# Performance work log

Hardware: AMD Instinct MI355X
Metric: run time of the kernel (lower is better)

Reference implementation:

```python
import jax, jax.numpy as jnp
import numpy as np

N_NODES = 200000
N_EDGES = 6400000
N_LAYERS = 3
Z_DIM = 4  # 2*4 + 1 + 3 == 12 == Linear in_features


def setup_inputs() -> dict:
    key = jax.random.key(0)
    ks = jax.random.split(key, 7)
    z = jax.random.normal(ks[0], (N_NODES, Z_DIM), dtype=jnp.float32)
    r = jax.random.uniform(ks[1], (N_EDGES, 1), dtype=jnp.float32)
    r_hat = jax.random.normal(ks[2], (N_EDGES, 3), dtype=jnp.float32)
    # Per-layer Linear(12, 1) weights and biases, stacked over layers.
    W = jax.random.normal(ks[3], (N_LAYERS, 1, 12), dtype=jnp.float32) * (1.0 / np.sqrt(12.0))
    b = jnp.zeros((N_LAYERS, 1), dtype=jnp.float32)
    src = jax.random.randint(ks[4], (N_EDGES,), 0, N_NODES, dtype=jnp.int32)
    dst = jax.random.randint(ks[5], (N_EDGES,), 0, N_NODES, dtype=jnp.int32)
    return {"z": z, "r": r, "r_hat": r_hat, "W": W, "b": b, "src": src, "dst": dst}


def reference(z, r, r_hat, W, b, src, dst):
    # batch['x'] = batch['z'].copy()
    x = z
    n_nodes = z.shape[0]
    for i in range(W.shape[0]):
        # Per-edge gather + concat -> [E, 12]
        inpt = jnp.concatenate([z[src], z[dst], r, r_hat], axis=-1)
        # Tiny Linear(12, 1) -> per-edge scalar message [E, 1]
        msg = inpt @ W[i].T + b[i]
        # Scatter-sum messages onto destination nodes, residual update.
        agg = jax.ops.segment_sum(msg, dst, num_segments=n_nodes)  # [N, 1]
        z = z + agg  # broadcast over the 4 node features
    return z, x
```

## Files before the change

kernel.cpp:

```cpp
#include <hip/hip_runtime.h>

#define N_NODES 200000
#define N_EDGES 6400000
#define K_BUCKETS 64
#define BUCKET 3125
#define NSB 3200
#define CHUNK 2000
#define P_SPLIT 8

__device__ __forceinline__ unsigned short f2bf(float x) {
    unsigned u = __float_as_uint(x);
    u += 0x7fffu + ((u >> 16) & 1u);
    return (unsigned short)(u >> 16);
}
__device__ __forceinline__ float bf2f(unsigned short h) {
    return __uint_as_float((unsigned)h << 16);
}


__global__ __launch_bounds__(256) void prep_kernel(
    const float4* __restrict__ z, float4* __restrict__ x_out,
    const float* __restrict__ W,
    float* __restrict__ u, float* __restrict__ v)
{
    int n = blockIdx.x * 256 + threadIdx.x;
    if (n >= N_NODES) return;
    float4 zv = z[n];
    x_out[n] = zv;
    float a0 = W[0], a1 = W[1], a2 = W[2], a3 = W[3];
    float q0 = W[4], q1 = W[5], q2 = W[6], q3 = W[7];
    u[n] = a0 * zv.x + a1 * zv.y + a2 * zv.z + a3 * zv.w;
    v[n] = q0 * zv.x + q1 * zv.y + q2 * zv.z + q3 * zv.w;
}

__global__ __launch_bounds__(256) void hist_kernel(const int* __restrict__ dst,
                                                   int* __restrict__ counts)
{
    __shared__ int cnt[K_BUCKETS];
    int tid = threadIdx.x, sb = blockIdx.x;
    if (tid < K_BUCKETS) cnt[tid] = 0;
    __syncthreads();
    int e0 = sb * CHUNK;
    for (int i = tid; i < CHUNK; i += 256)
        atomicAdd(&cnt[dst[e0 + i] / BUCKET], 1);
    __syncthreads();
    if (tid < K_BUCKETS) counts[sb * K_BUCKETS + tid] = cnt[tid];
}

__global__ __launch_bounds__(256) void scan_cols(const int* __restrict__ counts,
                                                 int* __restrict__ baseRel,
                                                 int* __restrict__ tot)
{
    __shared__ int buf[256];
    __shared__ int carry_s;
    int k = blockIdx.x, tid = threadIdx.x;
    if (tid == 0) carry_s = 0;
    __syncthreads();
    for (int base = 0; base < NSB; base += 256) {
        int idx = base + tid;
        int v = (idx < NSB) ? counts[idx * K_BUCKETS + k] : 0;
        buf[tid] = v;
        __syncthreads();
        for (int off = 1; off < 256; off <<= 1) {
            int t = (tid >= off) ? buf[tid - off] : 0;
            __syncthreads();
            buf[tid] += t;
            __syncthreads();
        }
        int incl = buf[tid];
        if (idx < NSB) baseRel[idx * K_BUCKETS + k] = carry_s + incl - v;
        __syncthreads();
        if (tid == 255) carry_s += incl;
        __syncthreads();
    }
    if (tid == 255) tot[k] = carry_s;
}

__global__ __launch_bounds__(64) void scan_tot(const int* __restrict__ tot,
                                               int* __restrict__ bstart)
{
    __shared__ int buf[K_BUCKETS];
    int tid = threadIdx.x;
    int v = tot[tid];
    buf[tid] = v;
    __syncthreads();
    for (int off = 1; off < K_BUCKETS; off <<= 1) {
        int t = (tid >= off) ? buf[tid - off] : 0;
        __syncthreads();
        buf[tid] += t;
        __syncthreads();
    }
    bstart[tid] = buf[tid] - v;
    if (tid == K_BUCKETS - 1) bstart[K_BUCKETS] = buf[tid];
}

__global__ __launch_bounds__(256) void scatter_kernel(
    const int* __restrict__ src, const int* __restrict__ dst,
    const float* __restrict__ r, const float* __restrict__ r_hat,
    const float* __restrict__ W, const float* __restrict__ b,
    const int* __restrict__ counts, const int* __restrict__ baseRel,
    const int* __restrict__ bstart,
    int* __restrict__ packedA, unsigned short* __restrict__ c0a,
    unsigned short* __restrict__ c1a, unsigned short* __restrict__ c2a)
{
    __shared__ int cur[K_BUCKETS];
    __shared__ int delta[K_BUCKETS];
    __shared__ int scanbuf[K_BUCKETS];
    __shared__ int            lpack[CHUNK];
    __shared__ unsigned short lc0[CHUNK];
    __shared__ unsigned short lc1[CHUNK];
    __shared__ unsigned short lc2[CHUNK];
    __shared__ unsigned char  skb[CHUNK];

    int tid = threadIdx.x, sb = blockIdx.x;

    if (tid < K_BUCKETS) {
        int v = counts[sb * K_BUCKETS + tid];
        scanbuf[tid] = v;
    }
    __syncthreads();
    for (int off = 1; off < K_BUCKETS; off <<= 1) {
        int t = 0;
        if (tid < K_BUCKETS && tid >= off) t = scanbuf[tid - off];
        __syncthreads();
        if (tid < K_BUCKETS) scanbuf[tid] += t;
        __syncthreads();
    }
    if (tid < K_BUCKETS) {
        int v = counts[sb * K_BUCKETS + tid];
        int localBase = scanbuf[tid] - v;
        int gBase = bstart[tid] + baseRel[sb * K_BUCKETS + tid];
        delta[tid] = gBase - localBase;
        cur[tid] = localBase;
    }
    __syncthreads();

    float w8_0 = W[8],  w9_0 = W[9],  w10_0 = W[10], w11_0 = W[11], b0 = b[0];
    float w8_1 = W[20], w9_1 = W[21], w10_1 = W[22], w11_1 = W[23], b1 = b[1];
    float w8_2 = W[32], w9_2 = W[33], w10_2 = W[34], w11_2 = W[35], b2 = b[2];

    int e0 = sb * CHUNK;
    for (int i = tid; i < CHUNK; i += 256) {
        int e = e0 + i;
        int d = dst[e];
        int k = d / BUCKET;
        int dl = d - k * BUCKET;
        int slot = atomicAdd(&cur[k], 1);
        int sn = src[e];
        float rv = r[e];
        size_t he = 3 * (size_t)e;
        float h0 = r_hat[he], h1 = r_hat[he + 1], h2 = r_hat[he + 2];
        lpack[slot] = (sn << 12) | dl;
        lc0[slot] = f2bf(w8_0 * rv + w9_0 * h0 + w10_0 * h1 + w11_0 * h2 + b0);
        lc1[slot] = f2bf(w8_1 * rv + w9_1 * h0 + w10_1 * h1 + w11_1 * h2 + b1);
        lc2[slot] = f2bf(w8_2 * rv + w9_2 * h0 + w10_2 * h1 + w11_2 * h2 + b2);
        skb[slot] = (unsigned char)k;
    }
    __syncthreads();

    for (int s = tid; s < CHUNK; s += 256) {
        int k = skb[s];
        int gpos = delta[k] + s;
        packedA[gpos] = lpack[s];
        c0a[gpos] = lc0[s];
        c1a[gpos] = lc1[s];
        c2a[gpos] = lc2[s];
    }
}

__global__ __launch_bounds__(1024) void pagg_kernel(
    const int* __restrict__ packedA, const unsigned short* __restrict__ ca,
    const int* __restrict__ bstart,
    const float* __restrict__ u, const float* __restrict__ v,
    float* __restrict__ partial)
{
    __shared__ float vsl[BUCKET];
    __shared__ float aggsl[BUCKET];
    int tid = threadIdx.x, blk = blockIdx.x;
    int k = blk / P_SPLIT;
    int p = blk - k * P_SPLIT;
    int nbase = k * BUCKET;

    for (int i = tid; i < BUCKET; i += 1024) {
        aggsl[i] = 0.0f;
        vsl[i] = v[nbase + i];
    }
    __syncthreads();

    int estart = bstart[k], eend = bstart[k + 1];
    int len = eend - estart;
    int per = (len + P_SPLIT - 1) / P_SPLIT;
    int lo = estart + p * per;
    int hi = min(lo + per, eend);

    for (int j = lo + tid; j < hi; j += 1024) {
        int pack = packedA[j];
        int s = pack >> 12;
        int dl = pack & 4095;
        float c = bf2f(ca[j]);
        unsafeAtomicAdd(&aggsl[dl], u[s] + vsl[dl] + c);
    }
    __syncthreads();

    float* pout = partial + (size_t)blk * BUCKET;
    for (int i = tid; i < BUCKET; i += 1024) pout[i] = aggsl[i];
}

__global__ __launch_bounds__(256) void fin_kernel(
    const float4* __restrict__ z0, const float* __restrict__ partial,
    const float* __restrict__ Sin, float* __restrict__ Sout,
    const float* __restrict__ W, int layer,
    float* __restrict__ u, float* __restrict__ v, float4* __restrict__ z_out)
{
    int n = blockIdx.x * 256 + threadIdx.x;
    if (n >= N_NODES) return;
    int k = n / BUCKET;
    int i = n - k * BUCKET;
    float agg = 0.0f;
    const float* pk = partial + (size_t)k * P_SPLIT * BUCKET + i;
#pragma unroll
    for (int p = 0; p < P_SPLIT; ++p) agg += pk[(size_t)p * BUCKET];
    float S = ((layer == 0) ? 0.0f : Sin[n]) + agg;
    if (layer < 2) {
        const float* Wn = W + 12 * (layer + 1);
        float a0 = Wn[0], a1 = Wn[1], a2 = Wn[2], a3 = Wn[3];
        float q0 = Wn[4], q1 = Wn[5], q2 = Wn[6], q3 = Wn[7];
        float A = a0 + a1 + a2 + a3, B = q0 + q1 + q2 + q3;
        float4 zv = z0[n];
        Sout[n] = S;
        u[n] = a0 * zv.x + a1 * zv.y + a2 * zv.z + a3 * zv.w + A * S;
        v[n] = q0 * zv.x + q1 * zv.y + q2 * zv.z + q3 * zv.w + B * S;
    } else {
        float4 zv = z0[n];
        zv.x += S; zv.y += S; zv.z += S; zv.w += S;
        z_out[n] = zv;
    }
}


__global__ __launch_bounds__(256) void init_kernel(
    const float4* __restrict__ z_in, float4* __restrict__ z_cur,
    float4* __restrict__ x_out, float* __restrict__ agg)
{
    int n = blockIdx.x * blockDim.x + threadIdx.x;
    if (n < N_NODES) {
        float4 vv = z_in[n];
        z_cur[n] = vv; x_out[n] = vv; agg[n] = 0.0f;
    }
}

__global__ __launch_bounds__(256) void edge_kernel(
    const float* __restrict__ z, const float* __restrict__ r,
    const float* __restrict__ r_hat, const int* __restrict__ src,
    const int* __restrict__ dst, const float* __restrict__ Wl,
    const float* __restrict__ bl, float* __restrict__ agg)
{
    int e = blockIdx.x * blockDim.x + threadIdx.x;
    if (e >= N_EDGES) return;
    float w0 = Wl[0], w1 = Wl[1], w2 = Wl[2], w3 = Wl[3];
    float w4 = Wl[4], w5 = Wl[5], w6 = Wl[6], w7 = Wl[7];
    float w8 = Wl[8], w9 = Wl[9], w10 = Wl[10], w11 = Wl[11];
    float bias = bl[0];
    int s = src[e], d = dst[e];
    float4 zs = ((const float4*)z)[s];
    float4 zd = ((const float4*)z)[d];
    float rv = r[e];
    const float* rh = r_hat + 3 * (size_t)e;
    float msg = w0*zs.x + w1*zs.y + w2*zs.z + w3*zs.w
              + w4*zd.x + w5*zd.y + w6*zd.z + w7*zd.w
              + w8*rv + w9*rh[0] + w10*rh[1] + w11*rh[2] + bias;
    unsafeAtomicAdd(&agg[d], msg);
}

__global__ __launch_bounds__(256) void node_update(float4* __restrict__ z_cur,
                                                   float* __restrict__ agg)
{
    int n = blockIdx.x * blockDim.x + threadIdx.x;
    if (n < N_NODES) {
        float a = agg[n]; float4 vv = z_cur[n];
        vv.x += a; vv.y += a; vv.z += a; vv.w += a;
        z_cur[n] = vv; agg[n] = 0.0f;
    }
}

__global__ __launch_bounds__(256) void final_update(const float4* __restrict__ z_cur,
                                                    const float* __restrict__ agg,
                                                    float4* __restrict__ z_out)
{
    int n = blockIdx.x * blockDim.x + threadIdx.x;
    if (n < N_NODES) {
        float a = agg[n]; float4 vv = z_cur[n];
        vv.x += a; vv.y += a; vv.z += a; vv.w += a;
        z_out[n] = vv;
    }
}


extern "C" void kernel_launch(void* const* d_in, const int* in_sizes, int n_in,
                              void* d_out, int out_size, void* d_ws, size_t ws_size,
                              hipStream_t stream)
{
    const float* z     = (const float*)d_in[0];
    const float* r     = (const float*)d_in[1];
    const float* r_hat = (const float*)d_in[2];
    const float* W     = (const float*)d_in[3];
    const float* b     = (const float*)d_in[4];
    const int*   src   = (const int*)d_in[5];
    const int*   dst   = (const int*)d_in[6];
    float* out = (float*)d_out;

    char* ws = (char*)d_ws;
    size_t off = 0;
    auto alloc = [&](size_t bytes) {
        void* p = ws + off;
        off += (bytes + 15) & ~(size_t)15;
        return p;
    };
    int*            packedA = (int*)alloc((size_t)N_EDGES * 4);
    unsigned short* c0a     = (unsigned short*)alloc((size_t)N_EDGES * 2);
    unsigned short* c1a     = (unsigned short*)alloc((size_t)N_EDGES * 2);
    unsigned short* c2a     = (unsigned short*)alloc((size_t)N_EDGES * 2);
    int*            counts  = (int*)alloc((size_t)NSB * K_BUCKETS * 4);
    int*            baseRel = (int*)alloc((size_t)NSB * K_BUCKETS * 4);
    int*            tot     = (int*)alloc((size_t)K_BUCKETS * 4);
    int*            bstart  = (int*)alloc((size_t)(K_BUCKETS + 1) * 4);
    float*          Sa      = (float*)alloc((size_t)N_NODES * 4);
    float*          Sb      = (float*)alloc((size_t)N_NODES * 4);
    float*          ubuf    = (float*)alloc((size_t)N_NODES * 4);
    float*          vbuf    = (float*)alloc((size_t)N_NODES * 4);
    float*          partial = (float*)alloc((size_t)K_BUCKETS * P_SPLIT * BUCKET * 4);
    size_t required = off;

    dim3 nblk((N_NODES + 255) / 256);

    if (ws_size >= required) {
        prep_kernel<<<nblk, 256, 0, stream>>>(
            (const float4*)z, (float4*)(out + 4 * (size_t)N_NODES), W, ubuf, vbuf);
        hist_kernel<<<NSB, 256, 0, stream>>>(dst, counts);
        scan_cols<<<K_BUCKETS, 256, 0, stream>>>(counts, baseRel, tot);
        scan_tot<<<1, 64, 0, stream>>>(tot, bstart);
        scatter_kernel<<<NSB, 256, 0, stream>>>(src, dst, r, r_hat, W, b,
                                                counts, baseRel, bstart,
                                                packedA, c0a, c1a, c2a);
        pagg_kernel<<<K_BUCKETS * P_SPLIT, 1024, 0, stream>>>(
            packedA, c0a, bstart, ubuf, vbuf, partial);
        fin_kernel<<<nblk, 256, 0, stream>>>(
            (const float4*)z, partial, Sa, Sa, W, 0, ubuf, vbuf, (float4*)out);
        pagg_kernel<<<K_BUCKETS * P_SPLIT, 1024, 0, stream>>>(
            packedA, c1a, bstart, ubuf, vbuf, partial);
        fin_kernel<<<nblk, 256, 0, stream>>>(
            (const float4*)z, partial, Sa, Sb, W, 1, ubuf, vbuf, (float4*)out);
        pagg_kernel<<<K_BUCKETS * P_SPLIT, 1024, 0, stream>>>(
            packedA, c2a, bstart, ubuf, vbuf, partial);
        fin_kernel<<<nblk, 256, 0, stream>>>(
            (const float4*)z, partial, Sb, Sb, W, 2, ubuf, vbuf, (float4*)out);
    } else {
        float* agg   = (float*)d_ws;
        float* z_cur = agg + N_NODES;
        dim3 eblk((N_EDGES + 255) / 256);
        init_kernel<<<nblk, 256, 0, stream>>>(
            (const float4*)z, (float4*)z_cur,
            (float4*)(out + 4 * (size_t)N_NODES), agg);
        for (int i = 0; i < 3; ++i) {
            edge_kernel<<<eblk, 256, 0, stream>>>(
                z_cur, r, r_hat, src, dst, W + 12 * i, b + i, agg);
            if (i < 2)
                node_update<<<nblk, 256, 0, stream>>>((float4*)z_cur, agg);
            else
                final_update<<<nblk, 256, 0, stream>>>(
                    (const float4*)z_cur, agg, (float4*)out);
        }
    }
}
```

Baseline: 373.6 us.

## Add second-level sort of edges by source bucket for gather locality

Adds a second counting-sort pass (histogram, scan, scatter) that reorders edges within each destination bucket by source-node bucket, so the u[s] gathers in the aggregation kernels hit nearby addresses. The partial-split factor is lowered from 8 to 4 when the extra workspace is available. This trades one extra full pass over the 6.4M edge arrays and more workspace for better cache locality across the three aggregation launches. A fallback keeps the old path when workspace is insufficient.

```diff
diff --git a/kernel.cpp b/kernel.cpp
--- a/kernel.cpp
+++ b/kernel.cpp
@@ -6,7 +6,7 @@
 #define BUCKET 3125
 #define NSB 3200
 #define CHUNK 2000
-#define P_SPLIT 8
+#define CPB 64
 
 __device__ __forceinline__ unsigned short f2bf(float x) {
     unsigned u = __float_as_uint(x);
@@ -114,10 +114,7 @@
 
     int tid = threadIdx.x, sb = blockIdx.x;
 
-    if (tid < K_BUCKETS) {
-        int v = counts[sb * K_BUCKETS + tid];
-        scanbuf[tid] = v;
-    }
+    if (tid < K_BUCKETS) scanbuf[tid] = counts[sb * K_BUCKETS + tid];
     __syncthreads();
     for (int off = 1; off < K_BUCKETS; off <<= 1) {
         int t = 0;
@@ -168,17 +165,132 @@
     }
 }
 
+
+__global__ __launch_bounds__(256) void hist2_kernel(
+    const int* __restrict__ packedA, const int* __restrict__ bstart,
+    int* __restrict__ counts2)
+{
+    __shared__ int cnt[K_BUCKETS];
+    int tid = threadIdx.x, blk = blockIdx.x;
+    int k = blk >> 6, ci = blk & 63;
+    if (tid < K_BUCKETS) cnt[tid] = 0;
+    __syncthreads();
+    int lo = bstart[k] + ci * CHUNK;
+    int hi = min(lo + CHUNK, bstart[k + 1]);
+    for (int j = lo + tid; j < hi; j += 256)
+        atomicAdd(&cnt[(packedA[j] >> 12) / BUCKET], 1);
+    __syncthreads();
+    if (tid < K_BUCKETS) counts2[blk * K_BUCKETS + tid] = cnt[tid];
+}
+
+__global__ __launch_bounds__(256) void scan2_kernel(
+    const int* __restrict__ counts2, int* __restrict__ baseRel2)
+{
+    __shared__ int m[CPB * K_BUCKETS];
+    __shared__ int colT[K_BUCKETS];
+    __shared__ int colB[K_BUCKETS];
+    int k = blockIdx.x, tid = threadIdx.x;
+    for (int i = tid; i < CPB * K_BUCKETS; i += 256)
+        m[i] = counts2[k * CPB * K_BUCKETS + i];
+    __syncthreads();
+    if (tid < K_BUCKETS) {
+        int s = tid, t = 0;
+        for (int ci = 0; ci < CPB; ++ci) {
+            int v = m[ci * K_BUCKETS + s];
+            m[ci * K_BUCKETS + s] = t;
+            t += v;
+        }
+        colT[s] = t;
+    }
+    __syncthreads();
+    if (tid == 0) {
+        int t = 0;
+        for (int s = 0; s < K_BUCKETS; ++s) { colB[s] = t; t += colT[s]; }
+    }
+    __syncthreads();
+    for (int i = tid; i < CPB * K_BUCKETS; i += 256) {
+        int s = i & 63;
+        baseRel2[k * CPB * K_BUCKETS + i] = colB[s] + m[i];
+    }
+}
+
+__global__ __launch_bounds__(256) void scatter2_kernel(
+    const int* __restrict__ packedA,
+    const unsigned short* __restrict__ c0a, const unsigned short* __restrict__ c1a,
+    const unsigned short* __restrict__ c2a,
+    const int* __restrict__ bstart, const int* __restrict__ counts2,
+    const int* __restrict__ baseRel2,
+    int* __restrict__ packedB,
+    unsigned short* __restrict__ c0b, unsigned short* __restrict__ c1b,
+    unsigned short* __restrict__ c2b)
+{
+    __shared__ int cur[K_BUCKETS];
+    __shared__ int delta[K_BUCKETS];
+    __shared__ int scanbuf[K_BUCKETS];
+    __shared__ int            lpack[CHUNK];
+    __shared__ unsigned short lc0[CHUNK];
+    __shared__ unsigned short lc1[CHUNK];
+    __shared__ unsigned short lc2[CHUNK];
+    __shared__ unsigned char  skb[CHUNK];
+
+    int tid = threadIdx.x, blk = blockIdx.x;
+    int k = blk >> 6, ci = blk & 63;
+    int lo = bstart[k] + ci * CHUNK;
+    int hi = min(lo + CHUNK, bstart[k + 1]);
+    int n = hi - lo;
+    if (n <= 0) return;
+
+    if (tid < K_BUCKETS) scanbuf[tid] = counts2[blk * K_BUCKETS + tid];
+    __syncthreads();
+    for (int off = 1; off < K_BUCKETS; off <<= 1) {
+        int t = 0;
+        if (tid < K_BUCKETS && tid >= off) t = scanbuf[tid - off];
+        __syncthreads();
+        if (tid < K_BUCKETS) scanbuf[tid] += t;
+        __syncthreads();
+    }
+    if (tid < K_BUCKETS) {
+        int v = counts2[blk * K_BUCKETS + tid];
+        int localBase = scanbuf[tid] - v;
+        int gBase = bstart[k] + baseRel2[blk * K_BUCKETS + tid];
+        delta[tid] = gBase - localBase;
+        cur[tid] = localBase;
+    }
+    __syncthreads();
+
+    for (int j = lo + tid; j < hi; j += 256) {
+        int pack = packedA[j];
+        int s = (pack >> 12) / BUCKET;
+        int slot = atomicAdd(&cur[s], 1);
+        lpack[slot] = pack;
+        lc0[slot] = c0a[j];
+        lc1[slot] = c1a[j];
+        lc2[slot] = c2a[j];
+        skb[slot] = (unsigned char)s;
+    }
+    __syncthreads();
+
+    for (int t = tid; t < n; t += 256) {
+        int s = skb[t];
+        int g = delta[s] + t;
+        packedB[g] = lpack[t];
+        c0b[g] = lc0[t];
+        c1b[g] = lc1[t];
+        c2b[g] = lc2[t];
+    }
+}
+
 __global__ __launch_bounds__(1024) void pagg_kernel(
-    const int* __restrict__ packedA, const unsigned short* __restrict__ ca,
+    const int* __restrict__ packed, const unsigned short* __restrict__ ca,
     const int* __restrict__ bstart,
     const float* __restrict__ u, const float* __restrict__ v,
-    float* __restrict__ partial)
+    float* __restrict__ partial, int ps)
 {
     __shared__ float vsl[BUCKET];
     __shared__ float aggsl[BUCKET];
     int tid = threadIdx.x, blk = blockIdx.x;
-    int k = blk / P_SPLIT;
-    int p = blk - k * P_SPLIT;
+    int k = blk / ps;
+    int p = blk - k * ps;
     int nbase = k * BUCKET;
 
     for (int i = tid; i < BUCKET; i += 1024) {
@@ -189,16 +301,15 @@
 
     int estart = bstart[k], eend = bstart[k + 1];
     int len = eend - estart;
-    int per = (len + P_SPLIT - 1) / P_SPLIT;
+    int per = (len + ps - 1) / ps;
     int lo = estart + p * per;
     int hi = min(lo + per, eend);
 
     for (int j = lo + tid; j < hi; j += 1024) {
-        int pack = packedA[j];
+        int pack = packed[j];
         int s = pack >> 12;
         int dl = pack & 4095;
-        float c = bf2f(ca[j]);
-        unsafeAtomicAdd(&aggsl[dl], u[s] + vsl[dl] + c);
+        unsafeAtomicAdd(&aggsl[dl], u[s] + vsl[dl] + bf2f(ca[j]));
     }
     __syncthreads();
 
@@ -209,7 +320,7 @@
 __global__ __launch_bounds__(256) void fin_kernel(
     const float4* __restrict__ z0, const float* __restrict__ partial,
     const float* __restrict__ Sin, float* __restrict__ Sout,
-    const float* __restrict__ W, int layer,
+    const float* __restrict__ W, int layer, int ps,
     float* __restrict__ u, float* __restrict__ v, float4* __restrict__ z_out)
 {
     int n = blockIdx.x * 256 + threadIdx.x;
@@ -217,9 +328,8 @@
     int k = n / BUCKET;
     int i = n - k * BUCKET;
     float agg = 0.0f;
-    const float* pk = partial + (size_t)k * P_SPLIT * BUCKET + i;
-#pragma unroll
-    for (int p = 0; p < P_SPLIT; ++p) agg += pk[(size_t)p * BUCKET];
+    const float* pk = partial + (size_t)k * ps * BUCKET + i;
+    for (int p = 0; p < ps; ++p) agg += pk[(size_t)p * BUCKET];
     float S = ((layer == 0) ? 0.0f : Sin[n]) + agg;
     if (layer < 2) {
         const float* Wn = W + 12 * (layer + 1);
@@ -328,12 +438,20 @@
     float*          Sb      = (float*)alloc((size_t)N_NODES * 4);
     float*          ubuf    = (float*)alloc((size_t)N_NODES * 4);
     float*          vbuf    = (float*)alloc((size_t)N_NODES * 4);
-    float*          partial = (float*)alloc((size_t)K_BUCKETS * P_SPLIT * BUCKET * 4);
-    size_t required = off;
+    float*          partial = (float*)alloc((size_t)K_BUCKETS * 8 * BUCKET * 4);
+    size_t requiredB = off;
+    int*            counts2  = (int*)alloc((size_t)K_BUCKETS * CPB * K_BUCKETS * 4);
+    int*            baseRel2 = (int*)alloc((size_t)K_BUCKETS * CPB * K_BUCKETS * 4);
+    int*            packedB  = (int*)alloc((size_t)N_EDGES * 4);
+    unsigned short* c0b      = (unsigned short*)alloc((size_t)N_EDGES * 2);
+    unsigned short* c1b      = (unsigned short*)alloc((size_t)N_EDGES * 2);
+    unsigned short* c2b      = (unsigned short*)alloc((size_t)N_EDGES * 2);
+    size_t requiredA = off;
 
     dim3 nblk((N_NODES + 255) / 256);
 
-    if (ws_size >= required) {
+    if (ws_size >= requiredB) {
+        bool tierA = (ws_size >= requiredA);
         prep_kernel<<<nblk, 256, 0, stream>>>(
             (const float4*)z, (float4*)(out + 4 * (size_t)N_NODES), W, ubuf, vbuf);
         hist_kernel<<<NSB, 256, 0, stream>>>(dst, counts);
@@ -342,18 +460,27 @@
         scatter_kernel<<<NSB, 256, 0, stream>>>(src, dst, r, r_hat, W, b,
                                                 counts, baseRel, bstart,
                                                 packedA, c0a, c1a, c2a);
-        pagg_kernel<<<K_BUCKETS * P_SPLIT, 1024, 0, stream>>>(
-            packedA, c0a, bstart, ubuf, vbuf, partial);
+        const int* pk = packedA;
+        const unsigned short *x0 = c0a, *x1 = c1a, *x2 = c2a;
+        int ps = 8;
+        if (tierA) {
+            hist2_kernel<<<K_BUCKETS * CPB, 256, 0, stream>>>(packedA, bstart, counts2);
+            scan2_kernel<<<K_BUCKETS, 256, 0, stream>>>(counts2, baseRel2);
+            scatter2_kernel<<<K_BUCKETS * CPB, 256, 0, stream>>>(
+                packedA, c0a, c1a, c2a, bstart, counts2, baseRel2,
+                packedB, c0b, c1b, c2b);
+            pk = packedB; x0 = c0b; x1 = c1b; x2 = c2b;
+            ps = 4;
+        }
+        pagg_kernel<<<K_BUCKETS * ps, 1024, 0, stream>>>(pk, x0, bstart, ubuf, vbuf, partial, ps);
         fin_kernel<<<nblk, 256, 0, stream>>>(
-            (const float4*)z, partial, Sa, Sa, W, 0, ubuf, vbuf, (float4*)out);
-        pagg_kernel<<<K_BUCKETS * P_SPLIT, 1024, 0, stream>>>(
-            packedA, c1a, bstart, ubuf, vbuf, partial);
+            (const float4*)z, partial, Sa, Sa, W, 0, ps, ubuf, vbuf, (float4*)out);
+        pagg_kernel<<<K_BUCKETS * ps, 1024, 0, stream>>>(pk, x1, bstart, ubuf, vbuf, partial, ps);
         fin_kernel<<<nblk, 256, 0, stream>>>(
-            (const float4*)z, partial, Sa, Sb, W, 1, ubuf, vbuf, (float4*)out);
-        pagg_kernel<<<K_BUCKETS * P_SPLIT, 1024, 0, stream>>>(
-            packedA, c2a, bstart, ubuf, vbuf, partial);
+            (const float4*)z, partial, Sa, Sb, W, 1, ps, ubuf, vbuf, (float4*)out);
+        pagg_kernel<<<K_BUCKETS * ps, 1024, 0, stream>>>(pk, x2, bstart, ubuf, vbuf, partial, ps);
         fin_kernel<<<nblk, 256, 0, stream>>>(
-            (const float4*)z, partial, Sb, Sb, W, 2, ubuf, vbuf, (float4*)out);
+            (const float4*)z, partial, Sb, Sb, W, 2, ps, ubuf, vbuf, (float4*)out);
     } else {
         float* agg   = (float*)d_ws;
         float* z_cur = agg + N_NODES;
```

Result: slower. 433.7 us (+16.1%).
